# Performance work log

Measured on AMD Instinct MI355X. Metric: run time of the kernel, lower is better.

The kernel has to match this reference:

```python
import jax, jax.numpy as jnp
import numpy as np

N_NODES = 50000
N_EDGES = 800000
HID = 256
EDGE_DIM = 3


def setup_inputs() -> dict:
    key = jax.random.key(0)
    ks = jax.random.split(key, 10)
    h = jax.random.normal(ks[0], (N_NODES, HID), dtype=jnp.float32)
    edge_index = jax.random.randint(ks[1], (2, N_EDGES), 0, N_NODES, dtype=jnp.int64)
    edge_attr = jax.random.normal(ks[2], (N_EDGES, EDGE_DIM), dtype=jnp.float32)
    # edge_mlp: Linear(3, hid//2) -> SiLU -> Linear(hid//2, 1)
    half = HID // 2
    W1 = jax.random.normal(ks[3], (EDGE_DIM, half), dtype=jnp.float32) / np.sqrt(EDGE_DIM)
    b1 = jnp.zeros((half,), dtype=jnp.float32)
    W2 = jax.random.normal(ks[4], (half, 1), dtype=jnp.float32) / np.sqrt(half)
    b2 = jnp.zeros((1,), dtype=jnp.float32)
    # GCNConv lin (bias=False inside lin; separate additive bias)
    Wc = jax.random.normal(ks[5], (HID, HID), dtype=jnp.float32) / np.sqrt(HID)
    bc = jnp.zeros((HID,), dtype=jnp.float32)
    return {"h": h, "edge_index": edge_index, "edge_attr": edge_attr,
            "W1": W1, "b1": b1, "W2": W2, "b2": b2, "Wc": Wc, "bc": bc}


def reference(h, edge_index, edge_attr, W1, b1, W2, b2, Wc, bc):
    N = h.shape[0]
    # per-edge scalar weight in (0,1): sigmoid(MLP(edge_attr))
    t = jax.nn.silu(edge_attr @ W1 + b1)
    w = jax.nn.sigmoid((t @ W2 + b2)[:, 0])  # [E]

    # add self loops with weight 1.0
    loop = jnp.arange(N, dtype=edge_index.dtype)
    row = jnp.concatenate([edge_index[0], loop])  # sources
    col = jnp.concatenate([edge_index[1], loop])  # targets
    ew = jnp.concatenate([w, jnp.ones((N,), dtype=w.dtype)])

    # symmetric normalization (PyG gcn_norm, flow source_to_target)
    deg = jax.ops.segment_sum(ew, col, num_segments=N)
    dinv = jnp.where(deg > 0, jax.lax.rsqrt(deg), 0.0)
    norm = dinv[row] * ew * dinv[col]  # [E+N]

    # linear transform then gather-scale-scatter aggregation
    x = h @ Wc  # [N, HID]
    msg = x[row] * norm[:, None]  # [E+N, HID]
    out = jax.ops.segment_sum(msg, col, num_segments=N) + bc
    return out
```

## Files before the change

kernel.cpp:

```cpp
#include <hip/hip_runtime.h>

#define NN 50000
#define NE 800000
#define HID 256
#define HALF 128
#define CAP 48
#define MT ((NN + 63) / 64)
#define MLPB (NE / 256)

typedef __attribute__((ext_vector_type(8))) short short8;
typedef __attribute__((ext_vector_type(4))) float floatx4;

#define QSCALE 5.9604644775390625e-8f

__device__ inline unsigned short f2b(float f) {
    unsigned int u = __float_as_uint(f);
    return (unsigned short)((u + 0x7FFFu + ((u >> 16) & 1u)) >> 16);
}
__device__ inline float b2f(unsigned int u) { return __uint_as_float(u << 16); }

__global__ __launch_bounds__(256) void k_prep(const float* __restrict__ Wc,
                                              unsigned short* __restrict__ Wt,
                                              uint4* __restrict__ zb) {
    int t = blockIdx.x * 256 + threadIdx.x;
    if (t < 25000) zb[t] = make_uint4(0u, 0u, 0u, 0u);
    int n = t >> 8, k = t & 255;
    Wt[n * 256 + k] = f2b(Wc[k * 256 + n]);
}

__global__ __launch_bounds__(256) void k_mlp_gemm(
    const float* __restrict__ A, const unsigned short* __restrict__ Wt,
    unsigned short* __restrict__ xh,
    const float* __restrict__ ea, const int* __restrict__ eidx,
    const float* __restrict__ W1, const float* __restrict__ b1,
    const float* __restrict__ W2, const float* __restrict__ b2,
    float* __restrict__ w, unsigned int* __restrict__ qs) {
    __shared__ __align__(16) unsigned char SMEM[40960];
    int tid = threadIdx.x;
    if (blockIdx.x < MT) {
        unsigned short* As = (unsigned short*)SMEM;
        int wave = tid >> 6, lane = tid & 63;
        int mbase = blockIdx.x * 64, nbase = wave * 64;
        int lrow = lane & 15, lg = lane >> 4;
        int srow = tid >> 2, skg = tid & 3;
        int arow = mbase + srow;
        if (arow >= NN) arow = NN - 1;
        const float* Ap = A + (size_t)arow * HID + skg * 8;

#define PACKST(c, f0, f1) { uint4 pk;                                   \
        pk.x = (unsigned)f2b(f0.x) | ((unsigned)f2b(f0.y) << 16);       \
        pk.y = (unsigned)f2b(f0.z) | ((unsigned)f2b(f0.w) << 16);       \
        pk.z = (unsigned)f2b(f1.x) | ((unsigned)f2b(f1.y) << 16);       \
        pk.w = (unsigned)f2b(f1.z) | ((unsigned)f2b(f1.w) << 16);       \
        *(uint4*)&As[(c) * 2560 + srow * 40 + skg * 8] = pk; }

#pragma unroll
        for (int g = 0; g < 2; ++g) {
            int c0 = g * 4;
            float4 fa0 = *(const float4*)(Ap + (c0 + 0) * 32);
            float4 fb0 = *(const float4*)(Ap + (c0 + 0) * 32 + 4);
            float4 fa1 = *(const float4*)(Ap + (c0 + 1) * 32);
            float4 fb1 = *(const float4*)(Ap + (c0 + 1) * 32 + 4);
            float4 fa2 = *(const float4*)(Ap + (c0 + 2) * 32);
            float4 fb2 = *(const float4*)(Ap + (c0 + 2) * 32 + 4);
            float4 fa3 = *(const float4*)(Ap + (c0 + 3) * 32);
            float4 fb3 = *(const float4*)(Ap + (c0 + 3) * 32 + 4);
            PACKST(c0 + 0, fa0, fb0);
            PACKST(c0 + 1, fa1, fb1);
            PACKST(c0 + 2, fa2, fb2);
            PACKST(c0 + 3, fa3, fb3);
        }
        __syncthreads();

        floatx4 acc[4][4];
#pragma unroll
        for (int t = 0; t < 4; ++t)
#pragma unroll
            for (int u = 0; u < 4; ++u)
                acc[t][u] = (floatx4){0.f, 0.f, 0.f, 0.f};

#pragma unroll
        for (int c = 0; c < 8; ++c) {
            short8 af[4], bf[4];
#pragma unroll
            for (int t = 0; t < 4; ++t)
                af[t] = *(const short8*)&As[c * 2560 + (t * 16 + lrow) * 40 + lg * 8];
#pragma unroll
            for (int u = 0; u < 4; ++u)
                bf[u] = *(const short8*)&Wt[(nbase + u * 16 + lrow) * 256 + c * 32 + lg * 8];
#pragma unroll
            for (int t = 0; t < 4; ++t)
#pragma unroll
                for (int u = 0; u < 4; ++u)
                    acc[t][u] = __builtin_amdgcn_mfma_f32_16x16x32_bf16(
                        af[t], bf[u], acc[t][u], 0, 0, 0);
        }
#pragma unroll
        for (int t = 0; t < 4; ++t) {
            int rowb = mbase + t * 16 + lg * 4;
#pragma unroll
            for (int r = 0; r < 4; ++r) {
                int row = rowb + r;
                if (row < NN) {
#pragma unroll
                    for (int u = 0; u < 4; ++u)
                        xh[row * 256 + nbase + u * 16 + lrow] = f2b(acc[t][u][r]);
                }
            }
        }
    } else {
        float4* wp = (float4*)SMEM;
        float* w2s = (float*)(SMEM + 2048);
        if (tid < HALF) {
            wp[tid] = make_float4(W1[tid], W1[HALF + tid], W1[2 * HALF + tid], b1[tid]);
            w2s[tid] = W2[tid];
        }
        __syncthreads();
        int e = (blockIdx.x - MT) * 256 + tid;
        if (e >= NE) return;
        float a0 = ea[3 * e], a1 = ea[3 * e + 1], a2 = ea[3 * e + 2];
        float acc = b2[0];
#pragma unroll 4
        for (int j = 0; j < HALF; ++j) {
            float4 wv = wp[j];
            float t = fmaf(a0, wv.x, fmaf(a1, wv.y, fmaf(a2, wv.z, wv.w)));
            float s = t * __builtin_amdgcn_rcpf(1.0f + __expf(-t));
            acc = fmaf(s, w2s[j], acc);
        }
        float wv = __builtin_amdgcn_rcpf(1.0f + __expf(-acc));
        w[e] = wv;
        int col = eidx[NE + e];
        atomicAdd(&qs[col], __float2uint_rn(wv * 16777216.0f));
    }
}

__global__ __launch_bounds__(256) void k_fill(
    const int* __restrict__ eidx, const float* __restrict__ w,
    const unsigned int* __restrict__ qs, unsigned int* __restrict__ cnt,
    unsigned int* __restrict__ epk) {
    int e = blockIdx.x * 256 + threadIdx.x;
    if (e >= NE) return;
    int row = eidx[e];
    int col = eidx[NE + e];
    unsigned slot = atomicAdd(&cnt[col], 1u);
    if (slot < CAP) {
        float dr = fmaf((float)qs[row], QSCALE, 1.0f);
        float dc = fmaf((float)qs[col], QSCALE, 1.0f);
        float nm = w[e] * rsqrtf(dr * dc);
        epk[col * CAP + slot] = (unsigned)row | ((unsigned)f2b(nm) << 16);
    }
}

__global__ __launch_bounds__(256) void k_aggregate(
    const unsigned short* __restrict__ xh, const unsigned int* __restrict__ cnt,
    const unsigned int* __restrict__ qs, const unsigned int* __restrict__ epk,
    const float* __restrict__ bc, float* __restrict__ out) {
    int n = blockIdx.x * 4 + (threadIdx.x >> 6);
    int lane = threadIdx.x & 63;
    if (n >= NN) return;
    int c4 = lane * 4;
    int cn = (int)cnt[n];
    if (cn > CAP) cn = CAP;
    float d = fmaf((float)qs[n], QSCALE, 1.0f);
    float s = __builtin_amdgcn_rcpf(d);
    ushort4 xv = *(const ushort4*)&xh[n * 256 + c4];
    float4 bv = *(const float4*)&bc[c4];
    float ax = fmaf(b2f(xv.x), s, bv.x);
    float ay = fmaf(b2f(xv.y), s, bv.y);
    float az = fmaf(b2f(xv.z), s, bv.z);
    float aw = fmaf(b2f(xv.w), s, bv.w);

    const uint4* bp = (const uint4*)(epk + n * CAP);
    int nb = (cn + 7) >> 3;
    uint4 qa = bp[0], qb = bp[1];
    for (int b = 0; b < nb; ++b) {
        int k0 = b * 8;
        int i2 = 2 * b + 2;
        if (i2 > 10) i2 = 10;
        uint4 qa2 = bp[i2], qb2 = bp[i2 + 1];
        unsigned p0 = (k0 + 0 < cn) ? qa.x : 0u;
        unsigned p1 = (k0 + 1 < cn) ? qa.y : 0u;
        unsigned p2 = (k0 + 2 < cn) ? qa.z : 0u;
        unsigned p3 = (k0 + 3 < cn) ? qa.w : 0u;
        unsigned p4 = (k0 + 4 < cn) ? qb.x : 0u;
        unsigned p5 = (k0 + 5 < cn) ? qb.y : 0u;
        unsigned p6 = (k0 + 6 < cn) ? qb.z : 0u;
        unsigned p7 = (k0 + 7 < cn) ? qb.w : 0u;
        ushort4 v0 = *(const ushort4*)&xh[(p0 & 0xFFFFu) * 256 + c4];
        ushort4 v1 = *(const ushort4*)&xh[(p1 & 0xFFFFu) * 256 + c4];
        ushort4 v2 = *(const ushort4*)&xh[(p2 & 0xFFFFu) * 256 + c4];
        ushort4 v3 = *(const ushort4*)&xh[(p3 & 0xFFFFu) * 256 + c4];
        ushort4 v4 = *(const ushort4*)&xh[(p4 & 0xFFFFu) * 256 + c4];
        ushort4 v5 = *(const ushort4*)&xh[(p5 & 0xFFFFu) * 256 + c4];
        ushort4 v6 = *(const ushort4*)&xh[(p6 & 0xFFFFu) * 256 + c4];
        ushort4 v7 = *(const ushort4*)&xh[(p7 & 0xFFFFu) * 256 + c4];
        float n0 = b2f(p0 >> 16), n1 = b2f(p1 >> 16);
        float n2 = b2f(p2 >> 16), n3 = b2f(p3 >> 16);
        float n4 = b2f(p4 >> 16), n5 = b2f(p5 >> 16);
        float n6 = b2f(p6 >> 16), n7 = b2f(p7 >> 16);
        ax = fmaf(b2f(v0.x), n0, ax); ay = fmaf(b2f(v0.y), n0, ay);
        az = fmaf(b2f(v0.z), n0, az); aw = fmaf(b2f(v0.w), n0, aw);
        ax = fmaf(b2f(v1.x), n1, ax); ay = fmaf(b2f(v1.y), n1, ay);
        az = fmaf(b2f(v1.z), n1, az); aw = fmaf(b2f(v1.w), n1, aw);
        ax = fmaf(b2f(v2.x), n2, ax); ay = fmaf(b2f(v2.y), n2, ay);
        az = fmaf(b2f(v2.z), n2, az); aw = fmaf(b2f(v2.w), n2, aw);
        ax = fmaf(b2f(v3.x), n3, ax); ay = fmaf(b2f(v3.y), n3, ay);
        az = fmaf(b2f(v3.z), n3, az); aw = fmaf(b2f(v3.w), n3, aw);
        ax = fmaf(b2f(v4.x), n4, ax); ay = fmaf(b2f(v4.y), n4, ay);
        az = fmaf(b2f(v4.z), n4, az); aw = fmaf(b2f(v4.w), n4, aw);
        ax = fmaf(b2f(v5.x), n5, ax); ay = fmaf(b2f(v5.y), n5, ay);
        az = fmaf(b2f(v5.z), n5, az); aw = fmaf(b2f(v5.w), n5, aw);
        ax = fmaf(b2f(v6.x), n6, ax); ay = fmaf(b2f(v6.y), n6, ay);
        az = fmaf(b2f(v6.z), n6, az); aw = fmaf(b2f(v6.w), n6, aw);
        ax = fmaf(b2f(v7.x), n7, ax); ay = fmaf(b2f(v7.y), n7, ay);
        az = fmaf(b2f(v7.z), n7, az); aw = fmaf(b2f(v7.w), n7, aw);
        qa = qa2; qb = qb2;
    }
    *(float4*)&out[n * 256 + c4] = make_float4(ax, ay, az, aw);
}

extern "C" void kernel_launch(void* const* d_in, const int* in_sizes, int n_in,
                              void* d_out, int out_size, void* d_ws, size_t ws_size,
                              hipStream_t stream) {
    const float* h   = (const float*)d_in[0];
    const int* eidx  = (const int*)d_in[1];
    const float* ea  = (const float*)d_in[2];
    const float* W1  = (const float*)d_in[3];
    const float* b1  = (const float*)d_in[4];
    const float* W2  = (const float*)d_in[5];
    const float* b2  = (const float*)d_in[6];
    const float* Wc  = (const float*)d_in[7];
    const float* bc  = (const float*)d_in[8];
    float* out = (float*)d_out;

    char* p = (char*)d_ws;
    float* w           = (float*)p;          p += (size_t)NE * 4;
    unsigned int* qs   = (unsigned int*)p;   p += (size_t)NN * 4;
    unsigned int* cnt  = (unsigned int*)p;   p += (size_t)NN * 4;
    unsigned int* epk  = (unsigned int*)p;   p += (size_t)NN * CAP * 4;
    unsigned short* xh = (unsigned short*)p; p += (size_t)NN * HID * 2;
    unsigned short* Wt = (unsigned short*)p;

    k_prep<<<256, 256, 0, stream>>>(Wc, Wt, (uint4*)qs);
    k_mlp_gemm<<<MT + MLPB, 256, 0, stream>>>(h, Wt, xh, ea, eidx,
                                              W1, b1, W2, b2, w, qs);
    k_fill<<<MLPB, 256, 0, stream>>>(eidx, w, qs, cnt, epk);
    k_aggregate<<<(NN + 3) / 4, 256, 0, stream>>>(xh, cnt, qs, epk, bc, out);
}
```

Before: 273.8 us.

## Fold source-side degree scaling into GEMM epilogue and fuse edge MLP with CSR fill

The symmetric normalization is split up. The source-side dinv is applied in the GEMM epilogue, so xs holds x*dinv. The target-side dinv is applied once per node at the end of aggregation. The edge MLP then writes the raw edge weight straight into the packed edge buffer, which removes the separate fill kernel and the w round-trip through memory. In exchange, the GEMM can no longer run concurrently with the MLP blocks, because it must wait for the degrees, and the extra bf16 rounding of x*dinv adds some numerical change.

```diff
diff --git a/kernel.cpp b/kernel.cpp
--- a/kernel.cpp
+++ b/kernel.cpp
@@ -6,7 +6,7 @@
 #define HALF 128
 #define CAP 48
 #define MT ((NN + 63) / 64)
-#define MLPB (NE / 256)
+#define MLPB ((NE + 255) / 256)
 
 typedef __attribute__((ext_vector_type(8))) short short8;
 typedef __attribute__((ext_vector_type(4))) float floatx4;
@@ -28,131 +28,119 @@
     Wt[n * 256 + k] = f2b(Wc[k * 256 + n]);
 }
 
-__global__ __launch_bounds__(256) void k_mlp_gemm(
-    const float* __restrict__ A, const unsigned short* __restrict__ Wt,
-    unsigned short* __restrict__ xh,
+__global__ __launch_bounds__(256) void k_mlp_fill(
     const float* __restrict__ ea, const int* __restrict__ eidx,
     const float* __restrict__ W1, const float* __restrict__ b1,
     const float* __restrict__ W2, const float* __restrict__ b2,
-    float* __restrict__ w, unsigned int* __restrict__ qs) {
-    __shared__ __align__(16) unsigned char SMEM[40960];
+    unsigned int* __restrict__ qs, unsigned int* __restrict__ cnt,
+    unsigned int* __restrict__ epk) {
+    __shared__ float4 wp[HALF];
+    __shared__ float w2s[HALF];
     int tid = threadIdx.x;
-    if (blockIdx.x < MT) {
-        unsigned short* As = (unsigned short*)SMEM;
-        int wave = tid >> 6, lane = tid & 63;
-        int mbase = blockIdx.x * 64, nbase = wave * 64;
-        int lrow = lane & 15, lg = lane >> 4;
-        int srow = tid >> 2, skg = tid & 3;
-        int arow = mbase + srow;
-        if (arow >= NN) arow = NN - 1;
-        const float* Ap = A + (size_t)arow * HID + skg * 8;
+    if (tid < HALF) {
+        wp[tid] = make_float4(W1[tid], W1[HALF + tid], W1[2 * HALF + tid], b1[tid]);
+        w2s[tid] = W2[tid];
+    }
+    __syncthreads();
+    int e = blockIdx.x * 256 + tid;
+    if (e >= NE) return;
+    float a0 = ea[3 * e], a1 = ea[3 * e + 1], a2 = ea[3 * e + 2];
+    float acc = b2[0];
+#pragma unroll 4
+    for (int j = 0; j < HALF; ++j) {
+        float4 wv = wp[j];
+        float t = fmaf(a0, wv.x, fmaf(a1, wv.y, fmaf(a2, wv.z, wv.w)));
+        float s = t * __builtin_amdgcn_rcpf(1.0f + __expf(-t));
+        acc = fmaf(s, w2s[j], acc);
+    }
+    float wv = __builtin_amdgcn_rcpf(1.0f + __expf(-acc));
+    int row = eidx[e];
+    int col = eidx[NE + e];
+    atomicAdd(&qs[col], __float2uint_rn(wv * 16777216.0f));
+    unsigned slot = atomicAdd(&cnt[col], 1u);
+    if (slot < CAP)
+        epk[col * CAP + slot] = (unsigned)row | ((unsigned)f2b(wv) << 16);
+}
+
+__global__ __launch_bounds__(256) void k_gemm(
+    const float* __restrict__ A, const unsigned short* __restrict__ Wt,
+    const unsigned int* __restrict__ qs, unsigned short* __restrict__ xs) {
+    __shared__ __align__(16) unsigned short As[8 * 64 * 40];
+    int tid = threadIdx.x;
+    int wave = tid >> 6, lane = tid & 63;
+    int mbase = blockIdx.x * 64, nbase = wave * 64;
+    int lrow = lane & 15, lg = lane >> 4;
+    int srow = tid >> 2, skg = tid & 3;
+    int arow = mbase + srow;
+    if (arow >= NN) arow = NN - 1;
+    const float* Ap = A + (size_t)arow * HID + skg * 8;
 
 #define PACKST(c, f0, f1) { uint4 pk;                                   \
-        pk.x = (unsigned)f2b(f0.x) | ((unsigned)f2b(f0.y) << 16);       \
-        pk.y = (unsigned)f2b(f0.z) | ((unsigned)f2b(f0.w) << 16);       \
-        pk.z = (unsigned)f2b(f1.x) | ((unsigned)f2b(f1.y) << 16);       \
-        pk.w = (unsigned)f2b(f1.z) | ((unsigned)f2b(f1.w) << 16);       \
-        *(uint4*)&As[(c) * 2560 + srow * 40 + skg * 8] = pk; }
-
-#pragma unroll
-        for (int g = 0; g < 2; ++g) {
-            int c0 = g * 4;
-            float4 fa0 = *(const float4*)(Ap + (c0 + 0) * 32);
-            float4 fb0 = *(const float4*)(Ap + (c0 + 0) * 32 + 4);
-            float4 fa1 = *(const float4*)(Ap + (c0 + 1) * 32);
-            float4 fb1 = *(const float4*)(Ap + (c0 + 1) * 32 + 4);
-            float4 fa2 = *(const float4*)(Ap + (c0 + 2) * 32);
-            float4 fb2 = *(const float4*)(Ap + (c0 + 2) * 32 + 4);
-            float4 fa3 = *(const float4*)(Ap + (c0 + 3) * 32);
-            float4 fb3 = *(const float4*)(Ap + (c0 + 3) * 32 + 4);
-            PACKST(c0 + 0, fa0, fb0);
-            PACKST(c0 + 1, fa1, fb1);
-            PACKST(c0 + 2, fa2, fb2);
-            PACKST(c0 + 3, fa3, fb3);
-        }
-        __syncthreads();
-
-        floatx4 acc[4][4];
+    pk.x = (unsigned)f2b(f0.x) | ((unsigned)f2b(f0.y) << 16);           \
+    pk.y = (unsigned)f2b(f0.z) | ((unsigned)f2b(f0.w) << 16);           \
+    pk.z = (unsigned)f2b(f1.x) | ((unsigned)f2b(f1.y) << 16);           \
+    pk.w = (unsigned)f2b(f1.z) | ((unsigned)f2b(f1.w) << 16);           \
+    *(uint4*)&As[(c) * 2560 + srow * 40 + skg * 8] = pk; }
+
+#pragma unroll
+    for (int g = 0; g < 2; ++g) {
+        int c0 = g * 4;
+        float4 fa0 = *(const float4*)(Ap + (c0 + 0) * 32);
+        float4 fb0 = *(const float4*)(Ap + (c0 + 0) * 32 + 4);
+        float4 fa1 = *(const float4*)(Ap + (c0 + 1) * 32);
+        float4 fb1 = *(const float4*)(Ap + (c0 + 1) * 32 + 4);
+        float4 fa2 = *(const float4*)(Ap + (c0 + 2) * 32);
+        float4 fb2 = *(const float4*)(Ap + (c0 + 2) * 32 + 4);
+        float4 fa3 = *(const float4*)(Ap + (c0 + 3) * 32);
+        float4 fb3 = *(const float4*)(Ap + (c0 + 3) * 32 + 4);
+        PACKST(c0 + 0, fa0, fb0);
+        PACKST(c0 + 1, fa1, fb1);
+        PACKST(c0 + 2, fa2, fb2);
+        PACKST(c0 + 3, fa3, fb3);
+    }
+    __syncthreads();
+
+    floatx4 acc[4][4];
+#pragma unroll
+    for (int t = 0; t < 4; ++t)
+#pragma unroll
+        for (int u = 0; u < 4; ++u)
+            acc[t][u] = (floatx4){0.f, 0.f, 0.f, 0.f};
+
+#pragma unroll
+    for (int c = 0; c < 8; ++c) {
+        short8 af[4], bf[4];
 #pragma unroll
         for (int t = 0; t < 4; ++t)
+            af[t] = *(const short8*)&As[c * 2560 + (t * 16 + lrow) * 40 + lg * 8];
+#pragma unroll
+        for (int u = 0; u < 4; ++u)
+            bf[u] = *(const short8*)&Wt[(nbase + u * 16 + lrow) * 256 + c * 32 + lg * 8];
+#pragma unroll
+        for (int t = 0; t < 4; ++t)
 #pragma unroll
             for (int u = 0; u < 4; ++u)
-                acc[t][u] = (floatx4){0.f, 0.f, 0.f, 0.f};
-
-#pragma unroll
-        for (int c = 0; c < 8; ++c) {
-            short8 af[4], bf[4];
-#pragma unroll
-            for (int t = 0; t < 4; ++t)
-                af[t] = *(const short8*)&As[c * 2560 + (t * 16 + lrow) * 40 + lg * 8];
-#pragma unroll
-            for (int u = 0; u < 4; ++u)
-                bf[u] = *(const short8*)&Wt[(nbase + u * 16 + lrow) * 256 + c * 32 + lg * 8];
-#pragma unroll
-            for (int t = 0; t < 4; ++t)
+                acc[t][u] = __builtin_amdgcn_mfma_f32_16x16x32_bf16(
+                    af[t], bf[u], acc[t][u], 0, 0, 0);
+    }
+#pragma unroll
+    for (int t = 0; t < 4; ++t) {
+        int rowb = mbase + t * 16 + lg * 4;
+#pragma unroll
+        for (int r = 0; r < 4; ++r) {
+            int row = rowb + r;
+            if (row < NN) {
+                float di = rsqrtf(fmaf((float)qs[row], QSCALE, 1.0f));
 #pragma unroll
                 for (int u = 0; u < 4; ++u)
-                    acc[t][u] = __builtin_amdgcn_mfma_f32_16x16x32_bf16(
-                        af[t], bf[u], acc[t][u], 0, 0, 0);
-        }
-#pragma unroll
-        for (int t = 0; t < 4; ++t) {
-            int rowb = mbase + t * 16 + lg * 4;
-#pragma unroll
-            for (int r = 0; r < 4; ++r) {
-                int row = rowb + r;
-                if (row < NN) {
-#pragma unroll
-                    for (int u = 0; u < 4; ++u)
-                        xh[row * 256 + nbase + u * 16 + lrow] = f2b(acc[t][u][r]);
-                }
+                    xs[row * 256 + nbase + u * 16 + lrow] = f2b(acc[t][u][r] * di);
             }
         }
-    } else {
-        float4* wp = (float4*)SMEM;
-        float* w2s = (float*)(SMEM + 2048);
-        if (tid < HALF) {
-            wp[tid] = make_float4(W1[tid], W1[HALF + tid], W1[2 * HALF + tid], b1[tid]);
-            w2s[tid] = W2[tid];
-        }
-        __syncthreads();
-        int e = (blockIdx.x - MT) * 256 + tid;
-        if (e >= NE) return;
-        float a0 = ea[3 * e], a1 = ea[3 * e + 1], a2 = ea[3 * e + 2];
-        float acc = b2[0];
-#pragma unroll 4
-        for (int j = 0; j < HALF; ++j) {
-            float4 wv = wp[j];
-            float t = fmaf(a0, wv.x, fmaf(a1, wv.y, fmaf(a2, wv.z, wv.w)));
-            float s = t * __builtin_amdgcn_rcpf(1.0f + __expf(-t));
-            acc = fmaf(s, w2s[j], acc);
-        }
-        float wv = __builtin_amdgcn_rcpf(1.0f + __expf(-acc));
-        w[e] = wv;
-        int col = eidx[NE + e];
-        atomicAdd(&qs[col], __float2uint_rn(wv * 16777216.0f));
-    }
-}
-
-__global__ __launch_bounds__(256) void k_fill(
-    const int* __restrict__ eidx, const float* __restrict__ w,
-    const unsigned int* __restrict__ qs, unsigned int* __restrict__ cnt,
-    unsigned int* __restrict__ epk) {
-    int e = blockIdx.x * 256 + threadIdx.x;
-    if (e >= NE) return;
-    int row = eidx[e];
-    int col = eidx[NE + e];
-    unsigned slot = atomicAdd(&cnt[col], 1u);
-    if (slot < CAP) {
-        float dr = fmaf((float)qs[row], QSCALE, 1.0f);
-        float dc = fmaf((float)qs[col], QSCALE, 1.0f);
-        float nm = w[e] * rsqrtf(dr * dc);
-        epk[col * CAP + slot] = (unsigned)row | ((unsigned)f2b(nm) << 16);
     }
 }
 
 __global__ __launch_bounds__(256) void k_aggregate(
-    const unsigned short* __restrict__ xh, const unsigned int* __restrict__ cnt,
+    const unsigned short* __restrict__ xs, const unsigned int* __restrict__ cnt,
     const unsigned int* __restrict__ qs, const unsigned int* __restrict__ epk,
     const float* __restrict__ bc, float* __restrict__ out) {
     int n = blockIdx.x * 4 + (threadIdx.x >> 6);
@@ -161,14 +149,9 @@
     int c4 = lane * 4;
     int cn = (int)cnt[n];
     if (cn > CAP) cn = CAP;
-    float d = fmaf((float)qs[n], QSCALE, 1.0f);
-    float s = __builtin_amdgcn_rcpf(d);
-    ushort4 xv = *(const ushort4*)&xh[n * 256 + c4];
-    float4 bv = *(const float4*)&bc[c4];
-    float ax = fmaf(b2f(xv.x), s, bv.x);
-    float ay = fmaf(b2f(xv.y), s, bv.y);
-    float az = fmaf(b2f(xv.z), s, bv.z);
-    float aw = fmaf(b2f(xv.w), s, bv.w);
+    float di = rsqrtf(fmaf((float)qs[n], QSCALE, 1.0f));
+    ushort4 xv = *(const ushort4*)&xs[n * 256 + c4];
+    float ax = b2f(xv.x), ay = b2f(xv.y), az = b2f(xv.z), aw = b2f(xv.w);
 
     const uint4* bp = (const uint4*)(epk + n * CAP);
     int nb = (cn + 7) >> 3;
@@ -186,14 +169,14 @@
         unsigned p5 = (k0 + 5 < cn) ? qb.y : 0u;
         unsigned p6 = (k0 + 6 < cn) ? qb.z : 0u;
         unsigned p7 = (k0 + 7 < cn) ? qb.w : 0u;
-        ushort4 v0 = *(const ushort4*)&xh[(p0 & 0xFFFFu) * 256 + c4];
-        ushort4 v1 = *(const ushort4*)&xh[(p1 & 0xFFFFu) * 256 + c4];
-        ushort4 v2 = *(const ushort4*)&xh[(p2 & 0xFFFFu) * 256 + c4];
-        ushort4 v3 = *(const ushort4*)&xh[(p3 & 0xFFFFu) * 256 + c4];
-        ushort4 v4 = *(const ushort4*)&xh[(p4 & 0xFFFFu) * 256 + c4];
-        ushort4 v5 = *(const ushort4*)&xh[(p5 & 0xFFFFu) * 256 + c4];
-        ushort4 v6 = *(const ushort4*)&xh[(p6 & 0xFFFFu) * 256 + c4];
-        ushort4 v7 = *(const ushort4*)&xh[(p7 & 0xFFFFu) * 256 + c4];
+        ushort4 v0 = *(const ushort4*)&xs[(p0 & 0xFFFFu) * 256 + c4];
+        ushort4 v1 = *(const ushort4*)&xs[(p1 & 0xFFFFu) * 256 + c4];
+        ushort4 v2 = *(const ushort4*)&xs[(p2 & 0xFFFFu) * 256 + c4];
+        ushort4 v3 = *(const ushort4*)&xs[(p3 & 0xFFFFu) * 256 + c4];
+        ushort4 v4 = *(const ushort4*)&xs[(p4 & 0xFFFFu) * 256 + c4];
+        ushort4 v5 = *(const ushort4*)&xs[(p5 & 0xFFFFu) * 256 + c4];
+        ushort4 v6 = *(const ushort4*)&xs[(p6 & 0xFFFFu) * 256 + c4];
+        ushort4 v7 = *(const ushort4*)&xs[(p7 & 0xFFFFu) * 256 + c4];
         float n0 = b2f(p0 >> 16), n1 = b2f(p1 >> 16);
         float n2 = b2f(p2 >> 16), n3 = b2f(p3 >> 16);
         float n4 = b2f(p4 >> 16), n5 = b2f(p5 >> 16);
@@ -216,7 +199,13 @@
         az = fmaf(b2f(v7.z), n7, az); aw = fmaf(b2f(v7.w), n7, aw);
         qa = qa2; qb = qb2;
     }
-    *(float4*)&out[n * 256 + c4] = make_float4(ax, ay, az, aw);
+    float4 bv = *(const float4*)&bc[c4];
+    float4 res;
+    res.x = fmaf(ax, di, bv.x);
+    res.y = fmaf(ay, di, bv.y);
+    res.z = fmaf(az, di, bv.z);
+    res.w = fmaf(aw, di, bv.w);
+    *(float4*)&out[n * 256 + c4] = res;
 }
 
 extern "C" void kernel_launch(void* const* d_in, const int* in_sizes, int n_in,
@@ -234,16 +223,14 @@
     float* out = (float*)d_out;
 
     char* p = (char*)d_ws;
-    float* w           = (float*)p;          p += (size_t)NE * 4;
     unsigned int* qs   = (unsigned int*)p;   p += (size_t)NN * 4;
     unsigned int* cnt  = (unsigned int*)p;   p += (size_t)NN * 4;
     unsigned int* epk  = (unsigned int*)p;   p += (size_t)NN * CAP * 4;
-    unsigned short* xh = (unsigned short*)p; p += (size_t)NN * HID * 2;
+    unsigned short* xs = (unsigned short*)p; p += (size_t)NN * HID * 2;
     unsigned short* Wt = (unsigned short*)p;
 
     k_prep<<<256, 256, 0, stream>>>(Wc, Wt, (uint4*)qs);
-    k_mlp_gemm<<<MT + MLPB, 256, 0, stream>>>(h, Wt, xh, ea, eidx,
-                                              W1, b1, W2, b2, w, qs);
-    k_fill<<<MLPB, 256, 0, stream>>>(eidx, w, qs, cnt, epk);
-    k_aggregate<<<(NN + 3) / 4, 256, 0, stream>>>(xh, cnt, qs, epk, bc, out);
-}
+    k_mlp_fill<<<MLPB, 256, 0, stream>>>(ea, eidx, W1, b1, W2, b2, qs, cnt, epk);
+    k_gemm<<<MT, 256, 0, stream>>>(h, Wt, qs, xs);
+    k_aggregate<<<(NN + 3) / 4, 256, 0, stream>>>(xs, cnt, qs, epk, bc, out);
+}
```

After: 277.2 us. No clear change (+1.3%).
